# Kernel optimization log

Measured on AMD Instinct MI355X. Metric: run time of the kernel, lower is better.

Reference implementation:

```python
import jax, jax.numpy as jnp
import numpy as np

D_MODEL = 1024


def _n2_features(N_tokens):
    # N = token + 1; matrix rows (flattened, row-major) per original build_n2_matrix:
    # [ (N-1)^2, N-1, N,
    #   (N-1)^2, 2N,  -1,
    #   (N-1)^2, 0,   2(N-0.5),
    #   (N-1)^2, 2(N-0.5), 0 ]
    t = N_tokens.astype(jnp.float32)          # t = N - 1
    t2 = t * t                                # (N-1)^2
    z = jnp.zeros_like(t)
    neg1 = -jnp.ones_like(t)
    two_t_p1 = 2.0 * t + 1.0                  # 2*(N-0.5)
    feats = jnp.stack(
        [t2, t, t + 1.0,
         t2, 2.0 * t + 2.0, neg1,
         t2, z, two_t_p1,
         t2, two_t_p1, z],
        axis=-1,
    )                                          # [B, S, 12]
    return feats


def setup_inputs() -> dict:
    key = jax.random.key(0)
    k_tok, k_w, k_b = jax.random.split(key, 3)
    N_tokens = jax.random.randint(k_tok, (4, 8192), 0, 32000, dtype=jnp.int64)
    # nn.Linear(12, d_model): weight [d_model, 12], bias [d_model]
    bound = 1.0 / np.sqrt(12.0)
    W = jax.random.uniform(k_w, (D_MODEL, 12), jnp.float32, -bound, bound)
    b = jax.random.uniform(k_b, (D_MODEL,), jnp.float32, -bound, bound)
    return {"N_tokens": N_tokens, "W": W, "b": b}


def reference(N_tokens, W, b):
    feats = _n2_features(N_tokens)             # [B, S, 12]
    return jnp.einsum('bsf,df->bsd', feats, W) + b
```

## Files before the change

### kernel.cpp

```cpp
#include <hip/hip_runtime.h>

#define D_MODEL 1024
#define TOKENS_PER_BLOCK 8

typedef float vfloat4 __attribute__((ext_vector_type(4)));

__global__ __launch_bounds__(256) void n2_embed_kernel(
    const int* __restrict__ toks,
    const float* __restrict__ W,
    const float* __restrict__ bias,
    float* __restrict__ out,
    int n_tokens)
{
    const int d0 = threadIdx.x * 4;

    float A[4], B[4], C[4];
#pragma unroll
    for (int j = 0; j < 4; ++j) {
        const float* w = W + (size_t)(d0 + j) * 12;
        float w0 = w[0], w1 = w[1], w2 = w[2], w3 = w[3];
        float w4 = w[4], w5 = w[5], w6 = w[6];
        float w8 = w[8], w9 = w[9], w10 = w[10];
        A[j] = (w0 + w3) + (w6 + w9);
        B[j] = w1 + w2 + 2.0f * w4 + 2.0f * w8 + 2.0f * w10;
        C[j] = w2 + 2.0f * w4 - w5 + w8 + w10 + bias[d0 + j];
    }

    const int tok_begin = blockIdx.x * TOKENS_PER_BLOCK;

    float tvals[TOKENS_PER_BLOCK];
#pragma unroll
    for (int i = 0; i < TOKENS_PER_BLOCK; ++i) {
        int tok = tok_begin + i;
        tvals[i] = (tok < n_tokens) ? (float)toks[tok] : 0.0f;
    }

#pragma unroll
    for (int i = 0; i < TOKENS_PER_BLOCK; ++i) {
        int tok = tok_begin + i;
        if (tok >= n_tokens) break;
        float t = tvals[i];
        float t2 = t * t;
        vfloat4 o;
        o.x = fmaf(t2, A[0], fmaf(t, B[0], C[0]));
        o.y = fmaf(t2, A[1], fmaf(t, B[1], C[1]));
        o.z = fmaf(t2, A[2], fmaf(t, B[2], C[2]));
        o.w = fmaf(t2, A[3], fmaf(t, B[3], C[3]));
        __builtin_nontemporal_store(o, (vfloat4*)(out + (size_t)tok * D_MODEL + d0));
    }
}

extern "C" void kernel_launch(void* const* d_in, const int* in_sizes, int n_in,
                              void* d_out, int out_size, void* d_ws, size_t ws_size,
                              hipStream_t stream) {
    const int* toks = (const int*)d_in[0];
    const float* W = (const float*)d_in[1];
    const float* bias = (const float*)d_in[2];
    float* out = (float*)d_out;

    int n_tokens = out_size / D_MODEL;
    int blocks = (n_tokens + TOKENS_PER_BLOCK - 1) / TOKENS_PER_BLOCK;

    n2_embed_kernel<<<blocks, 256, 0, stream>>>(toks, W, bias, out, n_tokens);
}
```

Before: 142.9 us.

## Precompute folded coefficients in a prologue kernel and double tokens per block

Splits the work into a one-block kernel that folds W and bias into three per-dimension coefficient vectors stored in workspace, plus a streaming kernel that loads those coefficients with vector loads. Tokens per block rise from 8 to 16, halving the block count and spreading the per-block setup over more output rows. The aim is to cut the redundant strided W reads each block did before. It adds a second launch and a dependency on workspace, and keeps a fallback fused path when no workspace is given.

```diff
diff --git a/kernel.cpp b/kernel.cpp
--- a/kernel.cpp
+++ b/kernel.cpp
@@ -1,11 +1,80 @@
 #include <hip/hip_runtime.h>
 
 #define D_MODEL 1024
-#define TOKENS_PER_BLOCK 8
+#define TPB_TOKENS 16
 
 typedef float vfloat4 __attribute__((ext_vector_type(4)));
 
-__global__ __launch_bounds__(256) void n2_embed_kernel(
+
+__global__ __launch_bounds__(256) void n2_coeffs_kernel(
+    const float* __restrict__ W,
+    const float* __restrict__ bias,
+    float* __restrict__ coeffs)
+{
+    const int d0 = threadIdx.x * 4;
+
+    float wv[48];
+    const vfloat4* wp = (const vfloat4*)(W + (size_t)d0 * 12);
+#pragma unroll
+    for (int k = 0; k < 12; ++k)
+        ((vfloat4*)wv)[k] = wp[k];
+
+    const vfloat4 bb = *(const vfloat4*)(bias + d0);
+
+    vfloat4 A, B, C;
+#pragma unroll
+    for (int j = 0; j < 4; ++j) {
+        const float* w = wv + j * 12;
+        float w0 = w[0], w1 = w[1], w2 = w[2], w3 = w[3];
+        float w4 = w[4], w5 = w[5], w6 = w[6];
+        float w8 = w[8], w9 = w[9], w10 = w[10];
+        A[j] = (w0 + w3) + (w6 + w9);
+        B[j] = w1 + w2 + 2.0f * w4 + 2.0f * w8 + 2.0f * w10;
+        C[j] = w2 + 2.0f * w4 - w5 + w8 + w10 + bb[j];
+    }
+
+    *(vfloat4*)(coeffs + d0)               = A;
+    *(vfloat4*)(coeffs + D_MODEL + d0)     = B;
+    *(vfloat4*)(coeffs + 2 * D_MODEL + d0) = C;
+}
+
+__global__ __launch_bounds__(256) void n2_embed_stream_kernel(
+    const int* __restrict__ toks,
+    const float* __restrict__ coeffs,
+    float* __restrict__ out,
+    int n_tokens)
+{
+    const int d0 = threadIdx.x * 4;
+
+    const vfloat4 A = *(const vfloat4*)(coeffs + d0);
+    const vfloat4 B = *(const vfloat4*)(coeffs + D_MODEL + d0);
+    const vfloat4 C = *(const vfloat4*)(coeffs + 2 * D_MODEL + d0);
+
+    const int tok_begin = blockIdx.x * TPB_TOKENS;
+
+    float tvals[TPB_TOKENS];
+#pragma unroll
+    for (int i = 0; i < TPB_TOKENS; ++i) {
+        int tok = tok_begin + i;
+        tvals[i] = (tok < n_tokens) ? (float)toks[tok] : 0.0f;
+    }
+
+#pragma unroll
+    for (int i = 0; i < TPB_TOKENS; ++i) {
+        int tok = tok_begin + i;
+        if (tok >= n_tokens) break;
+        float t = tvals[i];
+        float t2 = t * t;
+        vfloat4 o;
+        o.x = fmaf(t2, A.x, fmaf(t, B.x, C.x));
+        o.y = fmaf(t2, A.y, fmaf(t, B.y, C.y));
+        o.z = fmaf(t2, A.z, fmaf(t, B.z, C.z));
+        o.w = fmaf(t2, A.w, fmaf(t, B.w, C.w));
+        __builtin_nontemporal_store(o, (vfloat4*)(out + (size_t)tok * D_MODEL + d0));
+    }
+}
+
+__global__ __launch_bounds__(256) void n2_embed_fused_kernel(
     const int* __restrict__ toks,
     const float* __restrict__ W,
     const float* __restrict__ bias,
@@ -26,17 +95,16 @@
         C[j] = w2 + 2.0f * w4 - w5 + w8 + w10 + bias[d0 + j];
     }
 
-    const int tok_begin = blockIdx.x * TOKENS_PER_BLOCK;
-
-    float tvals[TOKENS_PER_BLOCK];
+    const int tok_begin = blockIdx.x * TPB_TOKENS;
+    float tvals[TPB_TOKENS];
 #pragma unroll
-    for (int i = 0; i < TOKENS_PER_BLOCK; ++i) {
+    for (int i = 0; i < TPB_TOKENS; ++i) {
         int tok = tok_begin + i;
         tvals[i] = (tok < n_tokens) ? (float)toks[tok] : 0.0f;
     }
 
 #pragma unroll
-    for (int i = 0; i < TOKENS_PER_BLOCK; ++i) {
+    for (int i = 0; i < TPB_TOKENS; ++i) {
         int tok = tok_begin + i;
         if (tok >= n_tokens) break;
         float t = tvals[i];
@@ -59,7 +127,13 @@
     float* out = (float*)d_out;
 
     int n_tokens = out_size / D_MODEL;
-    int blocks = (n_tokens + TOKENS_PER_BLOCK - 1) / TOKENS_PER_BLOCK;
+    int blocks = (n_tokens + TPB_TOKENS - 1) / TPB_TOKENS;
 
-    n2_embed_kernel<<<blocks, 256, 0, stream>>>(toks, W, bias, out, n_tokens);
+    if (d_ws != nullptr && ws_size >= 3 * D_MODEL * sizeof(float)) {
+        float* coeffs = (float*)d_ws;
+        n2_coeffs_kernel<<<1, 256, 0, stream>>>(W, bias, coeffs);
+        n2_embed_stream_kernel<<<blocks, 256, 0, stream>>>(toks, coeffs, out, n_tokens);
+    } else {
+        n2_embed_fused_kernel<<<blocks, 256, 0, stream>>>(toks, W, bias, out, n_tokens);
+    }
 }
```

Result: slower. 148.4 us (+3.9%).
